# Performance work log

Hardware: AMD Instinct MI355X
Metric: run time of the kernel (lower is better)

Reference implementation:

```python
import jax, jax.numpy as jnp
import numpy as np

N_NODES = 50000
N_EDGES = 800000
IN_FEATS = 64
HID_FEATS = 64


def setup_inputs() -> dict:
    key = jax.random.key(0)
    ks = jax.random.split(key, 5)
    x = jax.random.normal(ks[0], (N_NODES, IN_FEATS), dtype=jnp.float32)
    src = jax.random.randint(ks[1], (N_EDGES,), 0, N_NODES)
    dst = jax.random.randint(ks[2], (N_EDGES,), 0, N_NODES)
    # GraphConv parameters (Glorot-ish init, bias zeros as in dgl defaults)
    W1 = jax.random.normal(ks[3], (IN_FEATS, HID_FEATS), dtype=jnp.float32) / np.sqrt(IN_FEATS)
    b1 = jnp.zeros((HID_FEATS,), dtype=jnp.float32)
    W2 = jax.random.normal(ks[4], (HID_FEATS, IN_FEATS), dtype=jnp.float32) / np.sqrt(HID_FEATS)
    b2 = jnp.zeros((IN_FEATS,), dtype=jnp.float32)
    return {"x": x, "src": src, "dst": dst, "W1": W1, "b1": b1, "W2": W2, "b2": b2}


def _graph_conv(x, src, dst, W, b, n_nodes):
    """dgl GraphConv with norm='both': D_dst^{-1/2} A D_src^{-1/2} X W + b."""
    ones = jnp.ones((src.shape[0],), dtype=x.dtype)
    deg_out = jax.ops.segment_sum(ones, src, num_segments=n_nodes)
    deg_in = jax.ops.segment_sum(ones, dst, num_segments=n_nodes)
    norm_out = jnp.where(deg_out > 0, jax.lax.rsqrt(jnp.maximum(deg_out, 1.0)), 0.0)
    norm_in = jnp.where(deg_in > 0, jax.lax.rsqrt(jnp.maximum(deg_in, 1.0)), 0.0)
    h = x * norm_out[:, None]                                  # [N, F] scaled by src norm
    agg = jax.ops.segment_sum(h[src], dst, num_segments=n_nodes)  # gather over edges + scatter-add
    return (agg * norm_in[:, None]) @ W + b


def reference(x, src, dst, W1, b1, W2, b2):
    n, d = x.shape
    # dHdx: conv -> tanh -> conv
    y = jnp.tanh(_graph_conv(x, src, dst, W1, b1, n))
    y = _graph_conv(y, src, dst, W2, b2, n)
    # J = cat([I[d//2:], -I[:d//2]])  -> symplectic [[0, I], [-I, 0]]
    I = jnp.eye(d, dtype=x.dtype)
    J = jnp.concatenate([I[d // 2:], -I[: d // 2]], axis=0)
    # get_D is undefined in the source module; treated as zero dissipation term.
    return y @ J.T
```

## Files before the change

kernel.cpp:

```cpp
#include <hip/hip_runtime.h>
#include <hip/hip_bf16.h>
#include <math.h>

#define N_NODES 50000
#define N_EDGES 800000
#define F 64
#define NPAD 50048
#define NBLK ((N_NODES + 255) / 256)

#define P_HIST 256
#define CHUNK (N_EDGES / P_HIST)
#define WORDS8 12500
#define RBLK8 ((WORDS8 + 255) / 256)

#define LROW 36
#define LBLK ((N_NODES + 31) / 32)

typedef short short8 __attribute__((ext_vector_type(8)));
typedef float f32x4 __attribute__((ext_vector_type(4)));

__device__ inline unsigned short f2bf(float f) {
    unsigned u = __float_as_uint(f);
    unsigned r = (u + 0x7fffu + ((u >> 16) & 1u)) >> 16;
    return (unsigned short)r;
}
__device__ inline float bf2f(unsigned v) { return __uint_as_float(v << 16); }
__device__ inline float bf2f_hi(unsigned v) { return __uint_as_float(v & 0xffff0000u); }

__device__ inline unsigned wave_incl_scan(unsigned v, int lane) {
    #pragma unroll
    for (int d = 1; d < 64; d <<= 1) {
        unsigned u = __shfl_up(v, d, 64);
        if (lane >= d) v += u;
    }
    return v;
}


__global__ __launch_bounds__(256) void hist_kernel(
    const int* __restrict__ src, const int* __restrict__ dst,
    unsigned* __restrict__ histd, unsigned* __restrict__ hists)
{
    __shared__ unsigned lds[WORDS8];
    int p = blockIdx.x, t = threadIdx.x;
    int e0 = p * CHUNK;
    for (int hp = 0; hp < 2; ++hp) {
        const int* col = hp ? src : dst;
        unsigned* outp = (hp ? hists : histd) + (size_t)p * WORDS8;
        for (int i = t; i < WORDS8; i += 256) lds[i] = 0;
        __syncthreads();
        for (int i = t; i < CHUNK; i += 256) {
            int v = col[e0 + i];
            atomicAdd(&lds[v >> 2], 1u << ((v & 3) * 8));
        }
        __syncthreads();
        for (int i = t; i < WORDS8; i += 256) outp[i] = lds[i];
        __syncthreads();
    }
}

__global__ __launch_bounds__(256) void reduce_kernel(
    unsigned* __restrict__ histd, const unsigned* __restrict__ hists,
    float* __restrict__ norm_in, float* __restrict__ norm_out,
    int* __restrict__ row_off, unsigned* __restrict__ blockSums)
{
    __shared__ unsigned wsum[4];
    int t = threadIdx.x, b = blockIdx.x;
    int w = b * 256 + t;
    unsigned s0 = 0, s1 = 0, s2 = 0, s3 = 0;
    unsigned t0 = 0, t1 = 0, t2 = 0, t3 = 0;
    if (w < WORDS8) {
        for (int p = 0; p < P_HIST; ++p) {
            size_t idx = (size_t)p * WORDS8 + w;
            unsigned vd = histd[idx];
            histd[idx] = s0 | (s1 << 8) | (s2 << 16) | (s3 << 24);
            s0 += vd & 255u; s1 += (vd >> 8) & 255u;
            s2 += (vd >> 16) & 255u; s3 += vd >> 24;
            unsigned vs = hists[idx];
            t0 += vs & 255u; t1 += (vs >> 8) & 255u;
            t2 += (vs >> 16) & 255u; t3 += vs >> 24;
        }
        norm_in[4 * w]     = s0 ? rsqrtf((float)s0) : 0.f;
        norm_in[4 * w + 1] = s1 ? rsqrtf((float)s1) : 0.f;
        norm_in[4 * w + 2] = s2 ? rsqrtf((float)s2) : 0.f;
        norm_in[4 * w + 3] = s3 ? rsqrtf((float)s3) : 0.f;
        norm_out[4 * w]     = t0 ? rsqrtf((float)t0) : 0.f;
        norm_out[4 * w + 1] = t1 ? rsqrtf((float)t1) : 0.f;
        norm_out[4 * w + 2] = t2 ? rsqrtf((float)t2) : 0.f;
        norm_out[4 * w + 3] = t3 ? rsqrtf((float)t3) : 0.f;
    }
    unsigned quadsum = s0 + s1 + s2 + s3;
    int lane = t & 63, wid = t >> 6;
    unsigned inc = wave_incl_scan(quadsum, lane);
    if (lane == 63) wsum[wid] = inc;
    __syncthreads();
    if (t == 0) {
        unsigned acc = 0;
        #pragma unroll
        for (int q = 0; q < 4; ++q) { unsigned x = wsum[q]; wsum[q] = acc; acc += x; }
    }
    __syncthreads();
    unsigned excl = inc - quadsum + wsum[wid];
    if (w < WORDS8) {
        row_off[4 * w]     = (int)excl;
        row_off[4 * w + 1] = (int)(excl + s0);
        row_off[4 * w + 2] = (int)(excl + s0 + s1);
        row_off[4 * w + 3] = (int)(excl + s0 + s1 + s2);
    }
    if (t == 255) blockSums[b] = excl + quadsum;
}

__global__ __launch_bounds__(256) void scan_b_kernel(
    const unsigned* __restrict__ blockSums, unsigned* __restrict__ blockOff, int cnt)
{
    __shared__ unsigned wsum[4];
    int t = threadIdx.x;
    unsigned v = (t < cnt) ? blockSums[t] : 0u;
    int lane = t & 63, wid = t >> 6;
    unsigned inc = wave_incl_scan(v, lane);
    if (lane == 63) wsum[wid] = inc;
    __syncthreads();
    if (t == 0) {
        unsigned acc = 0;
        #pragma unroll
        for (int q = 0; q < 4; ++q) { unsigned x = wsum[q]; wsum[q] = acc; acc += x; }
    }
    __syncthreads();
    if (t < cnt) blockOff[t] = inc - v + wsum[wid];
}

__global__ __launch_bounds__(256) void scan_c2_kernel(
    const unsigned* __restrict__ blockOff, int* __restrict__ row_off)
{
    int t = threadIdx.x, b = blockIdx.x;
    int w = b * 256 + t;
    if (w < WORDS8) {
        int off = (int)blockOff[b];
        row_off[4 * w] += off;
        row_off[4 * w + 1] += off;
        row_off[4 * w + 2] += off;
        row_off[4 * w + 3] += off;
    }
    if (w == 0) row_off[N_NODES] = N_EDGES;
}

__global__ __launch_bounds__(256) void scatter_kernel(
    const int* __restrict__ src, const int* __restrict__ dst,
    const int* __restrict__ row_off, const unsigned* __restrict__ histd,
    int* __restrict__ csr_src)
{
    __shared__ unsigned lds[WORDS8];
    int p = blockIdx.x, t = threadIdx.x;
    int e0 = p * CHUNK;
    const unsigned* pref = histd + (size_t)p * WORDS8;
    for (int i = t; i < WORDS8; i += 256) lds[i] = 0;
    __syncthreads();
    for (int i = t; i < CHUNK; i += 256) {
        int d = dst[e0 + i];
        int sh = (d & 3) * 8;
        unsigned old = atomicAdd(&lds[d >> 2], 1u << sh);
        unsigned rank = (old >> sh) & 255u;
        unsigned pre  = (pref[d >> 2] >> sh) & 255u;
        csr_src[row_off[d] + (int)(pre + rank)] = src[e0 + i];
    }
}


__global__ __launch_bounds__(256) void degrees_kernel(
    const int* __restrict__ src, const int* __restrict__ dst,
    unsigned* __restrict__ deg_out_u, unsigned* __restrict__ deg_in_u)
{
    int e = blockIdx.x * 256 + threadIdx.x;
    if (e < N_EDGES) {
        atomicAdd(&deg_out_u[src[e]], 1u);
        atomicAdd(&deg_in_u[dst[e]], 1u);
    }
}

__global__ __launch_bounds__(256) void fb_scan_a_kernel(
    const unsigned* __restrict__ deg_in_u, const unsigned* __restrict__ deg_out_u,
    float* __restrict__ norm_out, float* __restrict__ norm_in,
    int* __restrict__ row_off, unsigned* __restrict__ blockSums)
{
    __shared__ unsigned wsum[4];
    int t = threadIdx.x, b = blockIdx.x;
    int idx = b * 256 + t;
    unsigned v = 0, dout = 0;
    if (idx < N_NODES) { v = deg_in_u[idx]; dout = deg_out_u[idx]; }
    int lane = t & 63, wid = t >> 6;
    unsigned inc = wave_incl_scan(v, lane);
    if (lane == 63) wsum[wid] = inc;
    __syncthreads();
    if (t == 0) {
        unsigned acc = 0;
        #pragma unroll
        for (int q = 0; q < 4; ++q) { unsigned x = wsum[q]; wsum[q] = acc; acc += x; }
    }
    __syncthreads();
    unsigned excl = inc - v + wsum[wid];
    if (idx < N_NODES) {
        row_off[idx] = (int)excl;
        norm_in[idx]  = v    ? rsqrtf((float)v)    : 0.f;
        norm_out[idx] = dout ? rsqrtf((float)dout) : 0.f;
    }
    if (t == 255) blockSums[b] = excl + v;
}

__global__ __launch_bounds__(256) void fb_scan_c_kernel(
    const unsigned* __restrict__ blockOff, int* __restrict__ row_off,
    unsigned* __restrict__ cursor)
{
    int idx = blockIdx.x * 256 + threadIdx.x;
    if (idx < N_NODES) {
        int v = row_off[idx] + (int)blockOff[blockIdx.x];
        row_off[idx] = v;
        cursor[idx] = (unsigned)v;
    }
    if (idx == 0) row_off[N_NODES] = N_EDGES;
}

__global__ __launch_bounds__(256) void fb_csr_fill_kernel(
    const int* __restrict__ src, const int* __restrict__ dst,
    unsigned* __restrict__ cursor, int* __restrict__ csr_src)
{
    int e = blockIdx.x * 256 + threadIdx.x;
    if (e < N_EDGES) {
        unsigned p = atomicAdd(&cursor[dst[e]], 1u);
        csr_src[p] = src[e];
    }
}


__global__ __launch_bounds__(256) void prescale_kernel(
    const float* __restrict__ x, const float* __restrict__ norm_out,
    unsigned* __restrict__ xb)
{
    int t = blockIdx.x * 256 + threadIdx.x;
    if (t < N_NODES * 32) {
        int n = t >> 5;
        float w = norm_out[n];
        float2 v = ((const float2*)x)[t];
        xb[t] = (unsigned)f2bf(v.x * w) | ((unsigned)f2bf(v.y * w) << 16);
    }
}

__device__ inline void block_agg32(
    const unsigned* __restrict__ tab, const float* __restrict__ norm_in,
    const int* __restrict__ row_off, const int* __restrict__ csr_src,
    int nb, unsigned* lds)
{
    int tid = threadIdx.x;
    int wid = tid >> 6, lane = tid & 63;
    int g = lane >> 3, lp = lane & 7;
    int m = wid * 8 + g;
    int n = nb + m;
    float a0 = 0.f, a1 = 0.f, a2 = 0.f, a3 = 0.f;
    float a4 = 0.f, a5 = 0.f, a6 = 0.f, a7 = 0.f;
    float w = 0.f;
    if (n < N_NODES) {
        int beg = row_off[n];
        int end = row_off[n + 1];
        w = norm_in[n];
        int e = beg;
        for (; e + 1 < end; e += 2) {
            int s0 = csr_src[e], s1 = csr_src[e + 1];
            uint4 v0 = *(const uint4*)(tab + (size_t)s0 * 32 + lp * 4);
            uint4 v1 = *(const uint4*)(tab + (size_t)s1 * 32 + lp * 4);
            a0 += bf2f(v0.x & 0xffffu); a1 += bf2f_hi(v0.x);
            a2 += bf2f(v0.y & 0xffffu); a3 += bf2f_hi(v0.y);
            a4 += bf2f(v0.z & 0xffffu); a5 += bf2f_hi(v0.z);
            a6 += bf2f(v0.w & 0xffffu); a7 += bf2f_hi(v0.w);
            a0 += bf2f(v1.x & 0xffffu); a1 += bf2f_hi(v1.x);
            a2 += bf2f(v1.y & 0xffffu); a3 += bf2f_hi(v1.y);
            a4 += bf2f(v1.z & 0xffffu); a5 += bf2f_hi(v1.z);
            a6 += bf2f(v1.w & 0xffffu); a7 += bf2f_hi(v1.w);
        }
        if (e < end) {
            int s0 = csr_src[e];
            uint4 v0 = *(const uint4*)(tab + (size_t)s0 * 32 + lp * 4);
            a0 += bf2f(v0.x & 0xffffu); a1 += bf2f_hi(v0.x);
            a2 += bf2f(v0.y & 0xffffu); a3 += bf2f_hi(v0.y);
            a4 += bf2f(v0.z & 0xffffu); a5 += bf2f_hi(v0.z);
            a6 += bf2f(v0.w & 0xffffu); a7 += bf2f_hi(v0.w);
        }
    }
    uint4 o;
    o.x = (unsigned)f2bf(a0 * w) | ((unsigned)f2bf(a1 * w) << 16);
    o.y = (unsigned)f2bf(a2 * w) | ((unsigned)f2bf(a3 * w) << 16);
    o.z = (unsigned)f2bf(a4 * w) | ((unsigned)f2bf(a5 * w) << 16);
    o.w = (unsigned)f2bf(a6 * w) | ((unsigned)f2bf(a7 * w) << 16);
    *(uint4*)(lds + m * LROW + lp * 4) = o;
}

__global__ __launch_bounds__(256) void layer1_fused_kernel(
    const unsigned* __restrict__ tab, const float* __restrict__ norm_in,
    const float* __restrict__ norm_out, const int* __restrict__ row_off,
    const int* __restrict__ csr_src, const float* __restrict__ Wm,
    const float* __restrict__ bias, unsigned short* __restrict__ hb)
{
    __shared__ unsigned lds[32 * LROW];
    int tid = threadIdx.x;
    int wid = tid >> 6, lane = tid & 63;
    int q = lane >> 4, lp16 = lane & 15;
    int nb = blockIdx.x * 32;

    short8 bfrag[2];
    #pragma unroll
    for (int kt = 0; kt < 2; ++kt)
        #pragma unroll
        for (int j = 0; j < 8; ++j)
            bfrag[kt][j] = (short)f2bf(Wm[(kt * 32 + q * 8 + j) * F + wid * 16 + lp16]);

    block_agg32(tab, norm_in, row_off, csr_src, nb, lds);
    __syncthreads();

    int nn = wid * 16 + lp16;
    float bv = bias[nn];
    #pragma unroll
    for (int rg = 0; rg < 2; ++rg) {
        short8 afrag[2];
        #pragma unroll
        for (int kt = 0; kt < 2; ++kt)
            afrag[kt] = *(const short8*)(lds + (rg * 16 + lp16) * LROW + kt * 16 + q * 4);
        f32x4 acc = (f32x4){0.f, 0.f, 0.f, 0.f};
        #pragma unroll
        for (int kt = 0; kt < 2; ++kt)
            acc = __builtin_amdgcn_mfma_f32_16x16x32_bf16(afrag[kt], bfrag[kt], acc, 0, 0, 0);
        #pragma unroll
        for (int r = 0; r < 4; ++r) {
            int row = nb + rg * 16 + q * 4 + r;
            if (row < N_NODES) {
                float z = tanhf(acc[r] + bv) * norm_out[row];
                hb[(size_t)row * F + nn] = f2bf(z);
            }
        }
    }
}

__global__ __launch_bounds__(256) void layer2_fused_kernel(
    const unsigned* __restrict__ tab, const float* __restrict__ norm_in,
    const int* __restrict__ row_off, const int* __restrict__ csr_src,
    const float* __restrict__ Wm, const float* __restrict__ bias,
    float* __restrict__ out)
{
    __shared__ unsigned lds[32 * LROW];
    int tid = threadIdx.x;
    int wid = tid >> 6, lane = tid & 63;
    int q = lane >> 4, lp16 = lane & 15;
    int nb = blockIdx.x * 32;

    short8 bfrag[2];
    #pragma unroll
    for (int kt = 0; kt < 2; ++kt)
        #pragma unroll
        for (int j = 0; j < 8; ++j)
            bfrag[kt][j] = (short)f2bf(Wm[(kt * 32 + q * 8 + j) * F + wid * 16 + lp16]);

    block_agg32(tab, norm_in, row_off, csr_src, nb, lds);
    __syncthreads();

    int nn = wid * 16 + lp16;
    float bv = bias[nn];
    int oc = (nn + 32) & 63;
    float sgn = (nn < 32) ? -1.f : 1.f;
    #pragma unroll
    for (int rg = 0; rg < 2; ++rg) {
        short8 afrag[2];
        #pragma unroll
        for (int kt = 0; kt < 2; ++kt)
            afrag[kt] = *(const short8*)(lds + (rg * 16 + lp16) * LROW + kt * 16 + q * 4);
        f32x4 acc = (f32x4){0.f, 0.f, 0.f, 0.f};
        #pragma unroll
        for (int kt = 0; kt < 2; ++kt)
            acc = __builtin_amdgcn_mfma_f32_16x16x32_bf16(afrag[kt], bfrag[kt], acc, 0, 0, 0);
        #pragma unroll
        for (int r = 0; r < 4; ++r) {
            int row = nb + rg * 16 + q * 4 + r;
            if (row < N_NODES) {
                float z = acc[r] + bv;
                out[(size_t)row * F + oc] = sgn * z;
            }
        }
    }
}

extern "C" void kernel_launch(void* const* d_in, const int* in_sizes, int n_in,
                              void* d_out, int out_size, void* d_ws, size_t ws_size,
                              hipStream_t stream) {
    const float* x   = (const float*)d_in[0];
    const int*   src = (const int*)d_in[1];
    const int*   dst = (const int*)d_in[2];
    const float* W1  = (const float*)d_in[3];
    const float* b1  = (const float*)d_in[4];
    const float* W2  = (const float*)d_in[5];
    const float* b2  = (const float*)d_in[6];
    float* out = (float*)d_out;

    unsigned* ws = (unsigned*)d_ws;
    float*    norm_out = (float*)ws;
    float*    norm_in  = (float*)(ws + NPAD);
    int*      row_off  = (int*)(ws + 2 * NPAD);
    int*      csr_src  = (int*)(ws + 3 * NPAD);
    unsigned* xb       = ws + 3 * NPAD + N_EDGES;
    unsigned* hbu      = xb + (size_t)NPAD * 32;
    unsigned* blockSums= hbu + (size_t)NPAD * 32;
    unsigned* blockOff = blockSums + 256;
    unsigned* tail     = blockOff + 256;
    unsigned* histd = tail;
    unsigned* hists = histd + (size_t)P_HIST * WORDS8;
    size_t need_new = ((size_t)(tail - ws) + 2 * (size_t)P_HIST * WORDS8) * 4;

    if (ws_size >= need_new) {
        hist_kernel<<<P_HIST, 256, 0, stream>>>(src, dst, histd, hists);
        reduce_kernel<<<RBLK8, 256, 0, stream>>>(histd, hists, norm_in, norm_out, row_off, blockSums);
        scan_b_kernel<<<1, 256, 0, stream>>>(blockSums, blockOff, RBLK8);
        scan_c2_kernel<<<RBLK8, 256, 0, stream>>>(blockOff, row_off);
        scatter_kernel<<<P_HIST, 256, 0, stream>>>(src, dst, row_off, histd, csr_src);
    } else {
        unsigned* deg_out_u = tail;
        unsigned* deg_in_u  = tail + NPAD;
        unsigned* cursor    = tail + 2 * NPAD;
        hipMemsetAsync(deg_out_u, 0, 2 * NPAD * sizeof(unsigned), stream);
        degrees_kernel<<<(N_EDGES + 255) / 256, 256, 0, stream>>>(src, dst, deg_out_u, deg_in_u);
        fb_scan_a_kernel<<<NBLK, 256, 0, stream>>>(deg_in_u, deg_out_u, norm_out, norm_in, row_off, blockSums);
        scan_b_kernel<<<1, 256, 0, stream>>>(blockSums, blockOff, NBLK);
        fb_scan_c_kernel<<<NBLK, 256, 0, stream>>>(blockOff, row_off, cursor);
        fb_csr_fill_kernel<<<(N_EDGES + 255) / 256, 256, 0, stream>>>(src, dst, cursor, csr_src);
    }

    prescale_kernel<<<(N_NODES * 32 + 255) / 256, 256, 0, stream>>>(x, norm_out, xb);
    layer1_fused_kernel<<<LBLK, 256, 0, stream>>>(
        xb, norm_in, norm_out, row_off, csr_src, W1, b1, (unsigned short*)hbu);

    layer2_fused_kernel<<<LBLK, 256, 0, stream>>>(
        hbu, norm_in, row_off, csr_src, W2, b2, out);
}
```

Measured before the change: 202.4 us.

## Parallelize histogram reduction across partitions with wave-level scans

```diff
diff --git a/kernel.cpp b/kernel.cpp
--- a/kernel.cpp
+++ b/kernel.cpp
@@ -59,39 +59,67 @@
     }
 }
 
-__global__ __launch_bounds__(256) void reduce_kernel(
+__global__ __launch_bounds__(256) void reduce_v2_kernel(
     unsigned* __restrict__ histd, const unsigned* __restrict__ hists,
     float* __restrict__ norm_in, float* __restrict__ norm_out,
-    int* __restrict__ row_off, unsigned* __restrict__ blockSums)
-{
-    __shared__ unsigned wsum[4];
-    int t = threadIdx.x, b = blockIdx.x;
-    int w = b * 256 + t;
-    unsigned s0 = 0, s1 = 0, s2 = 0, s3 = 0;
-    unsigned t0 = 0, t1 = 0, t2 = 0, t3 = 0;
-    if (w < WORDS8) {
-        for (int p = 0; p < P_HIST; ++p) {
-            size_t idx = (size_t)p * WORDS8 + w;
-            unsigned vd = histd[idx];
-            histd[idx] = s0 | (s1 << 8) | (s2 << 16) | (s3 << 24);
-            s0 += vd & 255u; s1 += (vd >> 8) & 255u;
-            s2 += (vd >> 16) & 255u; s3 += vd >> 24;
-            unsigned vs = hists[idx];
-            t0 += vs & 255u; t1 += (vs >> 8) & 255u;
-            t2 += (vs >> 16) & 255u; t3 += vs >> 24;
-        }
-        norm_in[4 * w]     = s0 ? rsqrtf((float)s0) : 0.f;
-        norm_in[4 * w + 1] = s1 ? rsqrtf((float)s1) : 0.f;
-        norm_in[4 * w + 2] = s2 ? rsqrtf((float)s2) : 0.f;
-        norm_in[4 * w + 3] = s3 ? rsqrtf((float)s3) : 0.f;
+    int* __restrict__ row_off, unsigned* __restrict__ wordsum)
+{
+    int tid = threadIdx.x;
+    int wid = tid >> 6, lane = tid & 63;
+    int w = blockIdx.x * 4 + wid;
+    unsigned h0 = histd[(size_t)(lane * 4 + 0) * WORDS8 + w];
+    unsigned h1 = histd[(size_t)(lane * 4 + 1) * WORDS8 + w];
+    unsigned h2 = histd[(size_t)(lane * 4 + 2) * WORDS8 + w];
+    unsigned h3 = histd[(size_t)(lane * 4 + 3) * WORDS8 + w];
+    unsigned lsum = h0 + h1 + h2 + h3;
+    unsigned inc = lsum;
+    #pragma unroll
+    for (int d = 1; d < 64; d <<= 1) {
+        unsigned u = __shfl_up(inc, d, 64);
+        if (lane >= d) inc += u;
+    }
+    unsigned run = inc - lsum;
+    histd[(size_t)(lane * 4 + 0) * WORDS8 + w] = run; run += h0;
+    histd[(size_t)(lane * 4 + 1) * WORDS8 + w] = run; run += h1;
+    histd[(size_t)(lane * 4 + 2) * WORDS8 + w] = run; run += h2;
+    histd[(size_t)(lane * 4 + 3) * WORDS8 + w] = run;
+    unsigned total = __shfl(inc, 63, 64);
+    unsigned s = hists[(size_t)(lane * 4 + 0) * WORDS8 + w]
+               + hists[(size_t)(lane * 4 + 1) * WORDS8 + w]
+               + hists[(size_t)(lane * 4 + 2) * WORDS8 + w]
+               + hists[(size_t)(lane * 4 + 3) * WORDS8 + w];
+    #pragma unroll
+    for (int d = 1; d < 64; d <<= 1) s += __shfl_xor(s, d, 64);
+    if (lane == 0) {
+        unsigned d0 = total & 255u, d1 = (total >> 8) & 255u;
+        unsigned d2 = (total >> 16) & 255u, d3 = total >> 24;
+        unsigned t0 = s & 255u, t1 = (s >> 8) & 255u;
+        unsigned t2 = (s >> 16) & 255u, t3 = s >> 24;
+        norm_in[4 * w]     = d0 ? rsqrtf((float)d0) : 0.f;
+        norm_in[4 * w + 1] = d1 ? rsqrtf((float)d1) : 0.f;
+        norm_in[4 * w + 2] = d2 ? rsqrtf((float)d2) : 0.f;
+        norm_in[4 * w + 3] = d3 ? rsqrtf((float)d3) : 0.f;
         norm_out[4 * w]     = t0 ? rsqrtf((float)t0) : 0.f;
         norm_out[4 * w + 1] = t1 ? rsqrtf((float)t1) : 0.f;
         norm_out[4 * w + 2] = t2 ? rsqrtf((float)t2) : 0.f;
         norm_out[4 * w + 3] = t3 ? rsqrtf((float)t3) : 0.f;
-    }
-    unsigned quadsum = s0 + s1 + s2 + s3;
+        int4 r;
+        r.x = 0; r.y = (int)d0; r.z = (int)(d0 + d1); r.w = (int)(d0 + d1 + d2);
+        *(int4*)(row_off + 4 * w) = r;
+        wordsum[w] = d0 + d1 + d2 + d3;
+    }
+}
+
+__global__ __launch_bounds__(256) void scanw_kernel(
+    const unsigned* __restrict__ wordsum, int* __restrict__ row_off,
+    unsigned* __restrict__ blockSums)
+{
+    __shared__ unsigned wsum[4];
+    int t = threadIdx.x, b = blockIdx.x;
+    int w = b * 256 + t;
+    unsigned v = (w < WORDS8) ? wordsum[w] : 0u;
     int lane = t & 63, wid = t >> 6;
-    unsigned inc = wave_incl_scan(quadsum, lane);
+    unsigned inc = wave_incl_scan(v, lane);
     if (lane == 63) wsum[wid] = inc;
     __syncthreads();
     if (t == 0) {
@@ -100,14 +128,13 @@
         for (int q = 0; q < 4; ++q) { unsigned x = wsum[q]; wsum[q] = acc; acc += x; }
     }
     __syncthreads();
-    unsigned excl = inc - quadsum + wsum[wid];
+    unsigned excl = inc - v + wsum[wid];
     if (w < WORDS8) {
-        row_off[4 * w]     = (int)excl;
-        row_off[4 * w + 1] = (int)(excl + s0);
-        row_off[4 * w + 2] = (int)(excl + s0 + s1);
-        row_off[4 * w + 3] = (int)(excl + s0 + s1 + s2);
-    }
-    if (t == 255) blockSums[b] = excl + quadsum;
+        int4 r = *(int4*)(row_off + 4 * w);
+        r.x += (int)excl; r.y += (int)excl; r.z += (int)excl; r.w += (int)excl;
+        *(int4*)(row_off + 4 * w) = r;
+    }
+    if (t == 255) blockSums[b] = excl + v;
 }
 
 __global__ __launch_bounds__(256) void scan_b_kernel(
@@ -136,10 +163,9 @@
     int w = b * 256 + t;
     if (w < WORDS8) {
         int off = (int)blockOff[b];
-        row_off[4 * w] += off;
-        row_off[4 * w + 1] += off;
-        row_off[4 * w + 2] += off;
-        row_off[4 * w + 3] += off;
+        int4 r = *(int4*)(row_off + 4 * w);
+        r.x += off; r.y += off; r.z += off; r.w += off;
+        *(int4*)(row_off + 4 * w) = r;
     }
     if (w == 0) row_off[N_NODES] = N_EDGES;
 }
@@ -405,14 +431,16 @@
     unsigned* hbu      = xb + (size_t)NPAD * 32;
     unsigned* blockSums= hbu + (size_t)NPAD * 32;
     unsigned* blockOff = blockSums + 256;
-    unsigned* tail     = blockOff + 256;
+    unsigned* wordsum  = blockOff + 256;
+    unsigned* tail     = wordsum + WORDS8;
     unsigned* histd = tail;
     unsigned* hists = histd + (size_t)P_HIST * WORDS8;
     size_t need_new = ((size_t)(tail - ws) + 2 * (size_t)P_HIST * WORDS8) * 4;
 
     if (ws_size >= need_new) {
         hist_kernel<<<P_HIST, 256, 0, stream>>>(src, dst, histd, hists);
-        reduce_kernel<<<RBLK8, 256, 0, stream>>>(histd, hists, norm_in, norm_out, row_off, blockSums);
+        reduce_v2_kernel<<<WORDS8 / 4, 256, 0, stream>>>(histd, hists, norm_in, norm_out, row_off, wordsum);
+        scanw_kernel<<<RBLK8, 256, 0, stream>>>(wordsum, row_off, blockSums);
         scan_b_kernel<<<1, 256, 0, stream>>>(blockSums, blockOff, RBLK8);
         scan_c2_kernel<<<RBLK8, 256, 0, stream>>>(blockOff, row_off);
         scatter_kernel<<<P_HIST, 256, 0, stream>>>(src, dst, row_off, histd, csr_src);
```

New measurement: 205.4 us. No clear change (+1.5%).
